# Optimization experiments

Measured on AMD Instinct MI355X. Metric: run time of the kernel, lower is better.

Reference implementation:

```python
import jax, jax.numpy as jnp
import numpy as np

N_NODES = 100000


def _gcn_conv(x, W, b, src, dst, norm):
    # x: [N, Fin] -> [N, Fout]; PyG GCNConv: linear, normalized scatter-add, bias
    x = x @ W
    msgs = x[src] * norm[:, None]  # gather + edge scale
    out = jax.ops.segment_sum(msgs, dst, num_segments=N_NODES)
    return out + b


def setup_inputs() -> dict:
    key = jax.random.key(0)
    ks = jax.random.split(key, 8)
    N, E, F, H, C = N_NODES, 600000, 128, 128, 40
    s = lambda fan: 1.0 / np.sqrt(fan)
    return {
        "features": jax.random.normal(ks[0], (N, F), dtype=jnp.float32),
        "edge_index": jax.random.randint(ks[1], (2, E), 0, N, dtype=jnp.int64),
        "W1": jax.random.normal(ks[2], (F, H), dtype=jnp.float32) * s(F),
        "b1": jnp.zeros((H,), dtype=jnp.float32),
        "W2": jax.random.normal(ks[3], (H, H), dtype=jnp.float32) * s(H),
        "b2": jnp.zeros((H,), dtype=jnp.float32),
        "W3": jax.random.normal(ks[4], (H, C), dtype=jnp.float32) * s(H),
        "b3": jnp.zeros((C,), dtype=jnp.float32),
    }


def reference(features, edge_index, W1, b1, W2, b2, W3, b3):
    N = N_NODES
    # add self-loops (PyG GCNConv default)
    loops = jnp.arange(N, dtype=edge_index.dtype)
    src = jnp.concatenate([edge_index[0], loops])
    dst = jnp.concatenate([edge_index[1], loops])
    # symmetric normalization: deg^-1/2[src] * deg^-1/2[dst]
    deg = jax.ops.segment_sum(jnp.ones_like(dst, dtype=features.dtype), dst,
                              num_segments=N)
    dis = jnp.where(deg > 0, jax.lax.rsqrt(jnp.maximum(deg, 1.0)), 0.0)
    norm = dis[src] * dis[dst]

    x = jax.nn.relu(_gcn_conv(features, W1, b1, src, dst, norm))
    x = jax.nn.relu(_gcn_conv(x, W2, b2, src, dst, norm))
    x = jax.nn.relu(_gcn_conv(x, W3, b3, src, dst, norm))
    return jax.nn.log_softmax(x, axis=-1)
```

## Files before the change

### kernel.cpp

```cpp
#include <hip/hip_runtime.h>
#include <hip/hip_bf16.h>

#define NN 100000
#define NE 600000
#define NBLK 391
#define NPAD 100096

typedef unsigned int uint;
typedef unsigned short ushort;
typedef __attribute__((ext_vector_type(8))) short bf16x8;
typedef __attribute__((ext_vector_type(4))) float f32x4;

__device__ __forceinline__ ushort f2b(float f) {
    union { float f; uint u; } v; v.f = f;
    return (ushort)((v.u + 0x7fffu + ((v.u >> 16) & 1u)) >> 16);
}
__device__ __forceinline__ uint f2b2(float lo, float hi) {
    return (uint)f2b(lo) | ((uint)f2b(hi) << 16);
}
__device__ __forceinline__ float b2f(uint h) {
    union { uint u; float f; } v; v.u = h << 16; return v.f;
}

__global__ __launch_bounds__(256) void k_cnt_init(int* __restrict__ cnt) {
    int i = blockIdx.x * 256 + threadIdx.x;
    if (i < NN) cnt[i] = 0;
}
__global__ __launch_bounds__(256) void k_cnt(const int* __restrict__ dst,
                                             int* __restrict__ cnt) {
    int e = blockIdx.x * 256 + threadIdx.x;
    if (e < NE) atomicAdd(&cnt[dst[e]], 1);
}
__global__ __launch_bounds__(256) void k_blockred(const int* __restrict__ cnt,
                                                  int* __restrict__ blocksum) {
    int t = threadIdx.x;
    int i = blockIdx.x * 256 + t;
    int c = (i < NN) ? cnt[i] : 0;
    #pragma unroll
    for (int o = 32; o; o >>= 1) c += __shfl_xor(c, o, 64);
    __shared__ int ws[4];
    if ((t & 63) == 0) ws[t >> 6] = c;
    __syncthreads();
    if (t == 0) blocksum[blockIdx.x] = ws[0] + ws[1] + ws[2] + ws[3];
}
__global__ __launch_bounds__(256) void k_scanblk_castW(const int* __restrict__ blocksum,
                                                       int* __restrict__ blockbase,
                                                       const float* __restrict__ W1,
                                                       const float* __restrict__ W2,
                                                       const float* __restrict__ W3,
                                                       ushort* __restrict__ WTall) {
    int t = threadIdx.x;
    if (blockIdx.x == 0) {
        __shared__ int s[NBLK];
        for (int i = t; i < NBLK; i += 256) s[i] = blocksum[i];
        __syncthreads();
        if (t == 0) {
            int run = 0;
            for (int i = 0; i < NBLK; ++i) { int v = s[i]; s[i] = run; run += v; }
        }
        __syncthreads();
        for (int i = t; i < NBLK; i += 256) blockbase[i] = s[i];
    } else {
        int o = (blockIdx.x - 1) * 256 + t;
        if (o >= 38912) return;
        float v;
        if (o < 32768) {
            const float* W = (o < 16384) ? W1 : W2;
            int off = o & 16383;
            int n = off >> 7, k = off & 127;
            v = W[k * 128 + n];
        } else {
            int off = o - 32768;
            int n = off >> 7, k = off & 127;
            v = (n < 40) ? W3[k * 40 + n] : 0.f;
        }
        WTall[o] = f2b(v);
    }
}
__global__ __launch_bounds__(256) void k_offsets(const int* __restrict__ cnt,
                                                 const int* __restrict__ blockbase,
                                                 int* __restrict__ offsets,
                                                 int* __restrict__ cursor,
                                                 float* __restrict__ dis) {
    int t = threadIdx.x, lane = t & 63, wv = t >> 6;
    int i = blockIdx.x * 256 + t;
    int c = (i < NN) ? cnt[i] : 0;
    int x = c;
    #pragma unroll
    for (int o = 1; o < 64; o <<= 1) {
        int v = __shfl_up(x, o, 64);
        if (lane >= o) x += v;
    }
    __shared__ int wsum[4], wbase[4];
    if (lane == 63) wsum[wv] = x;
    __syncthreads();
    if (t == 0) {
        int run = 0;
        #pragma unroll
        for (int k = 0; k < 4; ++k) { wbase[k] = run; run += wsum[k]; }
    }
    __syncthreads();
    int excl = blockbase[blockIdx.x] + wbase[wv] + x - c;
    if (i < NN) {
        offsets[i] = excl;
        cursor[i] = excl;
        dis[i] = rsqrtf((float)(c + 1));
        if (i == NN - 1) offsets[NN] = excl + c;
    }
}
__global__ __launch_bounds__(256) void k_fill(const int* __restrict__ src,
                                              const int* __restrict__ dst,
                                              const float* __restrict__ dis,
                                              int* __restrict__ cursor,
                                              int2* __restrict__ edges) {
    int e = blockIdx.x * 256 + threadIdx.x;
    if (e < NE) {
        int s = src[e], d = dst[e];
        int pos = atomicAdd(&cursor[d], 1);
        float nr = dis[s] * dis[d];
        edges[pos] = make_int2(s, __float_as_int(nr));
    }
}

template <bool F32IN>
__global__ __launch_bounds__(256) void k_gemm128b(const void* __restrict__ Xin,
                                                  const ushort* __restrict__ WT,
                                                  ushort* __restrict__ Yb) {
    __shared__ ushort AL[64 * 136];
    __shared__ ushort BL[128 * 136];
    const int t = threadIdx.x;
    const int rbase = blockIdx.x * 64;
    #pragma unroll
    for (int i = 0; i < 8; ++i) {
        int ch = t + 256 * i;
        int n = ch >> 4, c = ch & 15;
        *(int4*)(BL + n * 136 + c * 8) = *(const int4*)(WT + n * 128 + c * 8);
    }
    #pragma unroll
    for (int i = 0; i < 4; ++i) {
        int ch = t + 256 * i;
        int m = ch >> 4, c = ch & 15;
        int row = min(rbase + m, NN - 1);
        if (F32IN) {
            const float* Xf = (const float*)Xin;
            float4 f0 = *(const float4*)(Xf + (size_t)row * 128 + c * 8);
            float4 f1 = *(const float4*)(Xf + (size_t)row * 128 + c * 8 + 4);
            uint4 o;
            o.x = f2b2(f0.x, f0.y);
            o.y = f2b2(f0.z, f0.w);
            o.z = f2b2(f1.x, f1.y);
            o.w = f2b2(f1.z, f1.w);
            *(uint4*)(AL + m * 136 + c * 8) = o;
        } else {
            const ushort* Xb = (const ushort*)Xin;
            *(int4*)(AL + m * 136 + c * 8) =
                *(const int4*)(Xb + (size_t)row * 128 + c * 8);
        }
    }
    __syncthreads();
    const int wv = t >> 6, l = t & 63;
    const int m16 = l & 15, q = l >> 4;
    f32x4 acc[8];
    #pragma unroll
    for (int j = 0; j < 8; ++j) acc[j] = (f32x4){0.f, 0.f, 0.f, 0.f};
    #pragma unroll
    for (int kt = 0; kt < 4; ++kt) {
        bf16x8 a = *(const bf16x8*)(AL + (wv * 16 + m16) * 136 + kt * 32 + q * 8);
        #pragma unroll
        for (int j = 0; j < 8; ++j) {
            bf16x8 b = *(const bf16x8*)(BL + (j * 16 + m16) * 136 + kt * 32 + q * 8);
            acc[j] = __builtin_amdgcn_mfma_f32_16x16x32_bf16(a, b, acc[j], 0, 0, 0);
        }
    }
    #pragma unroll
    for (int r = 0; r < 4; ++r) {
        int row = rbase + wv * 16 + q * 4 + r;
        if (row < NN) {
            #pragma unroll
            for (int j = 0; j < 8; ++j)
                Yb[(size_t)row * 128 + j * 16 + m16] = f2b(acc[j][r]);
        }
    }
}

__global__ __launch_bounds__(256) void k_gemm40b(const ushort* __restrict__ Xb,
                                                 const ushort* __restrict__ W3T,
                                                 ushort* __restrict__ Yb) {
    __shared__ ushort AL[128 * 136];
    __shared__ ushort BL[48 * 136];
    const int t = threadIdx.x;
    const int rbase = blockIdx.x * 128;
    #pragma unroll
    for (int i = 0; i < 3; ++i) {
        int ch = t + 256 * i;
        int n = ch >> 4, c = ch & 15;
        *(int4*)(BL + n * 136 + c * 8) = *(const int4*)(W3T + n * 128 + c * 8);
    }
    #pragma unroll
    for (int i = 0; i < 8; ++i) {
        int ch = t + 256 * i;
        int m = ch >> 4, c = ch & 15;
        *(int4*)(AL + m * 136 + c * 8) =
            *(const int4*)(Xb + (size_t)(rbase + m) * 128 + c * 8);
    }
    __syncthreads();
    const int wv = t >> 6, l = t & 63;
    const int m16 = l & 15, q = l >> 4;
    f32x4 acc[2][3];
    #pragma unroll
    for (int i = 0; i < 2; ++i)
        #pragma unroll
        for (int j = 0; j < 3; ++j) acc[i][j] = (f32x4){0.f, 0.f, 0.f, 0.f};
    #pragma unroll
    for (int kt = 0; kt < 4; ++kt) {
        bf16x8 a[2], b[3];
        #pragma unroll
        for (int i = 0; i < 2; ++i)
            a[i] = *(const bf16x8*)(AL + ((wv * 2 + i) * 16 + m16) * 136 + kt * 32 + q * 8);
        #pragma unroll
        for (int j = 0; j < 3; ++j)
            b[j] = *(const bf16x8*)(BL + (j * 16 + m16) * 136 + kt * 32 + q * 8);
        #pragma unroll
        for (int i = 0; i < 2; ++i)
            #pragma unroll
            for (int j = 0; j < 3; ++j)
                acc[i][j] = __builtin_amdgcn_mfma_f32_16x16x32_bf16(a[i], b[j], acc[i][j], 0, 0, 0);
    }
    #pragma unroll
    for (int i = 0; i < 2; ++i) {
        #pragma unroll
        for (int r = 0; r < 4; ++r) {
            int row = rbase + (wv * 2 + i) * 16 + q * 4 + r;
            if (row < NN) {
                #pragma unroll
                for (int j = 0; j < 3; ++j)
                    Yb[(size_t)row * 64 + j * 16 + m16] = f2b(acc[i][j][r]);
            }
        }
    }
}

__global__ __launch_bounds__(256) void k_agg128b(const int* __restrict__ offsets,
                                                 const int2* __restrict__ edges,
                                                 const float* __restrict__ dis,
                                                 const ushort* __restrict__ xw,
                                                 const float* __restrict__ bias,
                                                 ushort* __restrict__ out) {
    const int t = threadIdx.x;
    const int wv = t >> 6, lane = t & 63;
    const int hl = lane & 15;
    const int qsel = lane & 48;
    const int n = (blockIdx.x * 4 + wv) * 4 + (lane >> 4);
    const bool nvalid = n < NN;
    const int nc = nvalid ? n : NN - 1;
    const int beg = offsets[nc], end = offsets[nc + 1];
    const int deg = end - beg;
    int2 em = (hl < deg) ? edges[beg + hl] : make_int2(0, 0);
    int s_l = em.x;
    float w_l = __int_as_float(em.y);
    float d = dis[nc];
    float dd = d * d;
    uint4 v0 = ((const uint4*)(xw + (size_t)nc * 128))[hl];
    float a0 = b2f(v0.x & 0xffffu) * dd, a1 = b2f(v0.x >> 16) * dd;
    float a2 = b2f(v0.y & 0xffffu) * dd, a3 = b2f(v0.y >> 16) * dd;
    float a4 = b2f(v0.z & 0xffffu) * dd, a5 = b2f(v0.z >> 16) * dd;
    float a6 = b2f(v0.w & 0xffffu) * dd, a7 = b2f(v0.w >> 16) * dd;
    int degc = min(deg, 16);
    int m1 = max(degc, __shfl_xor(degc, 16, 64));
    int dmax = max(m1, __shfl_xor(m1, 32, 64));
    int jceil = (dmax + 7) & ~7;
    for (int j = 0; j < jceil; j += 8) {
        int s[8]; float w[8]; uint4 u[8];
        #pragma unroll
        for (int k = 0; k < 8; ++k) {
            s[k] = __shfl(s_l, qsel + j + k, 64);
            w[k] = __shfl(w_l, qsel + j + k, 64);
        }
        #pragma unroll
        for (int k = 0; k < 8; ++k)
            u[k] = ((const uint4*)(xw + (size_t)s[k] * 128))[hl];
        #pragma unroll
        for (int k = 0; k < 8; ++k) {
            a0 = fmaf(b2f(u[k].x & 0xffffu), w[k], a0);
            a1 = fmaf(b2f(u[k].x >> 16), w[k], a1);
            a2 = fmaf(b2f(u[k].y & 0xffffu), w[k], a2);
            a3 = fmaf(b2f(u[k].y >> 16), w[k], a3);
            a4 = fmaf(b2f(u[k].z & 0xffffu), w[k], a4);
            a5 = fmaf(b2f(u[k].z >> 16), w[k], a5);
            a6 = fmaf(b2f(u[k].w & 0xffffu), w[k], a6);
            a7 = fmaf(b2f(u[k].w >> 16), w[k], a7);
        }
    }
    for (int jj = beg + 16; jj < end; ++jj) {
        int2 e2 = edges[jj];
        float w = __int_as_float(e2.y);
        uint4 u = ((const uint4*)(xw + (size_t)e2.x * 128))[hl];
        a0 = fmaf(b2f(u.x & 0xffffu), w, a0);
        a1 = fmaf(b2f(u.x >> 16), w, a1);
        a2 = fmaf(b2f(u.y & 0xffffu), w, a2);
        a3 = fmaf(b2f(u.y >> 16), w, a3);
        a4 = fmaf(b2f(u.z & 0xffffu), w, a4);
        a5 = fmaf(b2f(u.z >> 16), w, a5);
        a6 = fmaf(b2f(u.w & 0xffffu), w, a6);
        a7 = fmaf(b2f(u.w >> 16), w, a7);
    }
    float4 bv0 = ((const float4*)bias)[2 * hl];
    float4 bv1 = ((const float4*)bias)[2 * hl + 1];
    a0 = fmaxf(a0 + bv0.x, 0.f); a1 = fmaxf(a1 + bv0.y, 0.f);
    a2 = fmaxf(a2 + bv0.z, 0.f); a3 = fmaxf(a3 + bv0.w, 0.f);
    a4 = fmaxf(a4 + bv1.x, 0.f); a5 = fmaxf(a5 + bv1.y, 0.f);
    a6 = fmaxf(a6 + bv1.z, 0.f); a7 = fmaxf(a7 + bv1.w, 0.f);
    if (nvalid) {
        uint4 o;
        o.x = f2b2(a0, a1);
        o.y = f2b2(a2, a3);
        o.z = f2b2(a4, a5);
        o.w = f2b2(a6, a7);
        ((uint4*)(out + (size_t)n * 128))[hl] = o;
    }
}

__global__ __launch_bounds__(256) void k_agg40_lsm(const int* __restrict__ offsets,
                                                   const int2* __restrict__ edges,
                                                   const float* __restrict__ dis,
                                                   const ushort* __restrict__ xw,
                                                   const float* __restrict__ bias,
                                                   float* __restrict__ out) {
    const int t = threadIdx.x;
    const int wv = t >> 6, lane = t & 63;
    const int hl = lane & 31;
    const int hsel = lane & 32;
    const int n = (blockIdx.x * 4 + wv) * 2 + (lane >> 5);
    const bool nvalid = n < NN;
    const int nc = nvalid ? n : NN - 1;
    const bool act = hl < 20;
    const int beg = offsets[nc], end = offsets[nc + 1];
    const int deg = end - beg;
    int2 em = (hl < deg) ? edges[beg + hl] : make_int2(0, 0);
    int s_l = em.x;
    float w_l = __int_as_float(em.y);
    float d = dis[nc];
    uint v0 = ((const uint*)(xw + (size_t)nc * 64))[hl];
    float x0 = b2f(v0 & 0xffffu) * (d * d);
    float x1 = b2f(v0 >> 16) * (d * d);
    int degc = min(deg, 32);
    int dmax = max(degc, __shfl_xor(degc, 32, 64));
    int jceil = (dmax + 7) & ~7;
    for (int j = 0; j < jceil; j += 8) {
        int s[8]; float w[8]; uint u[8];
        #pragma unroll
        for (int k = 0; k < 8; ++k) {
            s[k] = __shfl(s_l, hsel + j + k, 64);
            w[k] = __shfl(w_l, hsel + j + k, 64);
        }
        #pragma unroll
        for (int k = 0; k < 8; ++k)
            u[k] = ((const uint*)(xw + (size_t)s[k] * 64))[hl];
        #pragma unroll
        for (int k = 0; k < 8; ++k) {
            x0 = fmaf(b2f(u[k] & 0xffffu), w[k], x0);
            x1 = fmaf(b2f(u[k] >> 16), w[k], x1);
        }
    }
    for (int jj = beg + 32; jj < end; ++jj) {
        int2 e2 = edges[jj];
        float w = __int_as_float(e2.y);
        uint u = ((const uint*)(xw + (size_t)e2.x * 64))[hl];
        x0 = fmaf(b2f(u & 0xffffu), w, x0);
        x1 = fmaf(b2f(u >> 16), w, x1);
    }
    if (act) {
        float2 bv = ((const float2*)bias)[hl];
        x0 = fmaxf(x0 + bv.x, 0.f);
        x1 = fmaxf(x1 + bv.y, 0.f);
    }
    float m = act ? fmaxf(x0, x1) : -1e30f;
    #pragma unroll
    for (int o = 16; o; o >>= 1) m = fmaxf(m, __shfl_xor(m, o, 64));
    float e = act ? (expf(x0 - m) + expf(x1 - m)) : 0.f;
    #pragma unroll
    for (int o = 16; o; o >>= 1) e += __shfl_xor(e, o, 64);
    if (act && nvalid) {
        float lg = m + logf(e);
        float2 o2 = make_float2(x0 - lg, x1 - lg);
        *(float2*)(out + (size_t)n * 40 + 2 * hl) = o2;
    }
}

extern "C" void kernel_launch(void* const* d_in, const int* in_sizes, int n_in,
                              void* d_out, int out_size, void* d_ws, size_t ws_size,
                              hipStream_t stream) {
    const float* feat = (const float*)d_in[0];
    const int* ei = (const int*)d_in[1];
    const float* W1 = (const float*)d_in[2];
    const float* b1 = (const float*)d_in[3];
    const float* W2 = (const float*)d_in[4];
    const float* b2 = (const float*)d_in[5];
    const float* W3 = (const float*)d_in[6];
    const float* b3 = (const float*)d_in[7];
    const int* src = ei;
    const int* dst = ei + NE;
    float* out = (float*)d_out;

    char* w = (char*)d_ws;
    int* cnt = (int*)w;        w += 100352 * 4;
    float* dis = (float*)w;    w += 100352 * 4;
    int* offsets = (int*)w;    w += 100608 * 4;
    int* cursor = (int*)w;     w += 100352 * 4;
    int* blocksum = (int*)w;   w += 512 * 4;
    int* blockbase = (int*)w;  w += 512 * 4;
    int2* edges = (int2*)w;    w += 600064 * 8;
    ushort* WTall = (ushort*)w; w += 39168 * 2;
    ushort* W1T = WTall;
    ushort* W2T = WTall + 16384;
    ushort* W3T = WTall + 32768;
    ushort* bufYb = (ushort*)w; w += (size_t)NPAD * 128 * 2;
    ushort* bufXb = (ushort*)w; w += (size_t)NPAD * 128 * 2;
    ushort* Y40b = (ushort*)w;  w += (size_t)NPAD * 64 * 2;

    const int B = 256;
    #define CDIV(a, b) (((a) + (b) - 1) / (b))

    k_cnt_init<<<NBLK, B, 0, stream>>>(cnt);
    k_cnt<<<CDIV(NE, B), B, 0, stream>>>(dst, cnt);
    k_blockred<<<NBLK, B, 0, stream>>>(cnt, blocksum);
    k_scanblk_castW<<<1 + CDIV(38912, B), B, 0, stream>>>(blocksum, blockbase,
                                                          W1, W2, W3, WTall);
    k_offsets<<<NBLK, B, 0, stream>>>(cnt, blockbase, offsets, cursor, dis);
    k_fill<<<CDIV(NE, B), B, 0, stream>>>(src, dst, dis, cursor, edges);

    k_gemm128b<true><<<CDIV(NN, 64), B, 0, stream>>>(feat, W1T, bufYb);
    k_agg128b<<<CDIV(NN, 16), B, 0, stream>>>(offsets, edges, dis, bufYb, b1, bufXb);
    k_gemm128b<false><<<CDIV(NN, 64), B, 0, stream>>>(bufXb, W2T, bufYb);
    k_agg128b<<<CDIV(NN, 16), B, 0, stream>>>(offsets, edges, dis, bufYb, b2, bufXb);
    k_gemm40b<<<CDIV(NN, 128), B, 0, stream>>>(bufXb, W3T, Y40b);
    k_agg40_lsm<<<CDIV(NN, 8), B, 0, stream>>>(offsets, edges, dis, Y40b, b3, out);
    #undef CDIV
}
```

Baseline: 278.6 us.

## Fold source normalization into GEMM epilogue and drop per-edge weights

Factors the symmetric norm so each GEMM output row is pre-scaled by deg^-1/2 of its own node, and the destination factor is applied once after aggregation. The CSR then stores only source indices (4 bytes per edge instead of 8), so the gather loops become plain adds with no per-edge weight shuffles. CSR fill now uses the rank returned by the counting atomic instead of a second atomic cursor pass. A zero row at index NN is written so padded lanes can gather it safely. The cost is an extra rank array and a per-row dis load in the GEMM epilogues; rounding to bf16 now happens after scaling by dis, which shifts numerics slightly.

```diff
diff --git a/kernel.cpp b/kernel.cpp
--- a/kernel.cpp
+++ b/kernel.cpp
@@ -27,9 +27,10 @@
     if (i < NN) cnt[i] = 0;
 }
 __global__ __launch_bounds__(256) void k_cnt(const int* __restrict__ dst,
-                                             int* __restrict__ cnt) {
+                                             int* __restrict__ cnt,
+                                             int* __restrict__ rank) {
     int e = blockIdx.x * 256 + threadIdx.x;
-    if (e < NE) atomicAdd(&cnt[dst[e]], 1);
+    if (e < NE) rank[e] = atomicAdd(&cnt[dst[e]], 1);
 }
 __global__ __launch_bounds__(256) void k_blockred(const int* __restrict__ cnt,
                                                   int* __restrict__ blocksum) {
@@ -80,7 +81,6 @@
 __global__ __launch_bounds__(256) void k_offsets(const int* __restrict__ cnt,
                                                  const int* __restrict__ blockbase,
                                                  int* __restrict__ offsets,
-                                                 int* __restrict__ cursor,
                                                  float* __restrict__ dis) {
     int t = threadIdx.x, lane = t & 63, wv = t >> 6;
     int i = blockIdx.x * 256 + t;
@@ -103,33 +103,35 @@
     int excl = blockbase[blockIdx.x] + wbase[wv] + x - c;
     if (i < NN) {
         offsets[i] = excl;
-        cursor[i] = excl;
         dis[i] = rsqrtf((float)(c + 1));
         if (i == NN - 1) offsets[NN] = excl + c;
     }
 }
 __global__ __launch_bounds__(256) void k_fill(const int* __restrict__ src,
                                               const int* __restrict__ dst,
-                                              const float* __restrict__ dis,
-                                              int* __restrict__ cursor,
-                                              int2* __restrict__ edges) {
+                                              const int* __restrict__ rank,
+                                              const int* __restrict__ offsets,
+                                              int* __restrict__ edges) {
     int e = blockIdx.x * 256 + threadIdx.x;
     if (e < NE) {
-        int s = src[e], d = dst[e];
-        int pos = atomicAdd(&cursor[d], 1);
-        float nr = dis[s] * dis[d];
-        edges[pos] = make_int2(s, __float_as_int(nr));
+        int s = src[e], d = dst[e], r = rank[e];
+        edges[offsets[d] + r] = s;
     }
 }
 
 template <bool F32IN>
 __global__ __launch_bounds__(256) void k_gemm128b(const void* __restrict__ Xin,
                                                   const ushort* __restrict__ WT,
+                                                  const float* __restrict__ dis,
                                                   ushort* __restrict__ Yb) {
     __shared__ ushort AL[64 * 136];
     __shared__ ushort BL[128 * 136];
     const int t = threadIdx.x;
     const int rbase = blockIdx.x * 64;
+    if (blockIdx.x == 0 && t < 16) {
+        uint4 z = make_uint4(0, 0, 0, 0);
+        ((uint4*)(Yb + (size_t)NN * 128))[t] = z;
+    }
     #pragma unroll
     for (int i = 0; i < 8; ++i) {
         int ch = t + 256 * i;
@@ -176,20 +178,26 @@
     for (int r = 0; r < 4; ++r) {
         int row = rbase + wv * 16 + q * 4 + r;
         if (row < NN) {
+            float ds = dis[row];
             #pragma unroll
             for (int j = 0; j < 8; ++j)
-                Yb[(size_t)row * 128 + j * 16 + m16] = f2b(acc[j][r]);
+                Yb[(size_t)row * 128 + j * 16 + m16] = f2b(acc[j][r] * ds);
         }
     }
 }
 
 __global__ __launch_bounds__(256) void k_gemm40b(const ushort* __restrict__ Xb,
                                                  const ushort* __restrict__ W3T,
+                                                 const float* __restrict__ dis,
                                                  ushort* __restrict__ Yb) {
     __shared__ ushort AL[128 * 136];
     __shared__ ushort BL[48 * 136];
     const int t = threadIdx.x;
     const int rbase = blockIdx.x * 128;
+    if (blockIdx.x == 0 && t < 8) {
+        uint4 z = make_uint4(0, 0, 0, 0);
+        ((uint4*)(Yb + (size_t)NN * 64))[t] = z;
+    }
     #pragma unroll
     for (int i = 0; i < 3; ++i) {
         int ch = t + 256 * i;
@@ -200,8 +208,9 @@
     for (int i = 0; i < 8; ++i) {
         int ch = t + 256 * i;
         int m = ch >> 4, c = ch & 15;
+        int row = min(rbase + m, NN - 1);
         *(int4*)(AL + m * 136 + c * 8) =
-            *(const int4*)(Xb + (size_t)(rbase + m) * 128 + c * 8);
+            *(const int4*)(Xb + (size_t)row * 128 + c * 8);
     }
     __syncthreads();
     const int wv = t >> 6, l = t & 63;
@@ -232,16 +241,17 @@
         for (int r = 0; r < 4; ++r) {
             int row = rbase + (wv * 2 + i) * 16 + q * 4 + r;
             if (row < NN) {
+                float ds = dis[row];
                 #pragma unroll
                 for (int j = 0; j < 3; ++j)
-                    Yb[(size_t)row * 64 + j * 16 + m16] = f2b(acc[i][j][r]);
+                    Yb[(size_t)row * 64 + j * 16 + m16] = f2b(acc[i][j][r] * ds);
             }
         }
     }
 }
 
 __global__ __launch_bounds__(256) void k_agg128b(const int* __restrict__ offsets,
-                                                 const int2* __restrict__ edges,
+                                                 const int* __restrict__ edges,
                                                  const float* __restrict__ dis,
                                                  const ushort* __restrict__ xw,
                                                  const float* __restrict__ bias,
@@ -255,61 +265,46 @@
     const int nc = nvalid ? n : NN - 1;
     const int beg = offsets[nc], end = offsets[nc + 1];
     const int deg = end - beg;
-    int2 em = (hl < deg) ? edges[beg + hl] : make_int2(0, 0);
-    int s_l = em.x;
-    float w_l = __int_as_float(em.y);
-    float d = dis[nc];
-    float dd = d * d;
+    int s_l = (hl < deg) ? edges[beg + hl] : NN;
     uint4 v0 = ((const uint4*)(xw + (size_t)nc * 128))[hl];
-    float a0 = b2f(v0.x & 0xffffu) * dd, a1 = b2f(v0.x >> 16) * dd;
-    float a2 = b2f(v0.y & 0xffffu) * dd, a3 = b2f(v0.y >> 16) * dd;
-    float a4 = b2f(v0.z & 0xffffu) * dd, a5 = b2f(v0.z >> 16) * dd;
-    float a6 = b2f(v0.w & 0xffffu) * dd, a7 = b2f(v0.w >> 16) * dd;
+    float a0 = b2f(v0.x & 0xffffu), a1 = b2f(v0.x >> 16);
+    float a2 = b2f(v0.y & 0xffffu), a3 = b2f(v0.y >> 16);
+    float a4 = b2f(v0.z & 0xffffu), a5 = b2f(v0.z >> 16);
+    float a6 = b2f(v0.w & 0xffffu), a7 = b2f(v0.w >> 16);
     int degc = min(deg, 16);
     int m1 = max(degc, __shfl_xor(degc, 16, 64));
     int dmax = max(m1, __shfl_xor(m1, 32, 64));
     int jceil = (dmax + 7) & ~7;
     for (int j = 0; j < jceil; j += 8) {
-        int s[8]; float w[8]; uint4 u[8];
-        #pragma unroll
-        for (int k = 0; k < 8; ++k) {
-            s[k] = __shfl(s_l, qsel + j + k, 64);
-            w[k] = __shfl(w_l, qsel + j + k, 64);
-        }
+        int s[8]; uint4 u[8];
+        #pragma unroll
+        for (int k = 0; k < 8; ++k) s[k] = __shfl(s_l, qsel + j + k, 64);
         #pragma unroll
         for (int k = 0; k < 8; ++k)
             u[k] = ((const uint4*)(xw + (size_t)s[k] * 128))[hl];
         #pragma unroll
         for (int k = 0; k < 8; ++k) {
-            a0 = fmaf(b2f(u[k].x & 0xffffu), w[k], a0);
-            a1 = fmaf(b2f(u[k].x >> 16), w[k], a1);
-            a2 = fmaf(b2f(u[k].y & 0xffffu), w[k], a2);
-            a3 = fmaf(b2f(u[k].y >> 16), w[k], a3);
-            a4 = fmaf(b2f(u[k].z & 0xffffu), w[k], a4);
-            a5 = fmaf(b2f(u[k].z >> 16), w[k], a5);
-            a6 = fmaf(b2f(u[k].w & 0xffffu), w[k], a6);
-            a7 = fmaf(b2f(u[k].w >> 16), w[k], a7);
+            a0 += b2f(u[k].x & 0xffffu); a1 += b2f(u[k].x >> 16);
+            a2 += b2f(u[k].y & 0xffffu); a3 += b2f(u[k].y >> 16);
+            a4 += b2f(u[k].z & 0xffffu); a5 += b2f(u[k].z >> 16);
+            a6 += b2f(u[k].w & 0xffffu); a7 += b2f(u[k].w >> 16);
         }
     }
     for (int jj = beg + 16; jj < end; ++jj) {
-        int2 e2 = edges[jj];
-        float w = __int_as_float(e2.y);
-        uint4 u = ((const uint4*)(xw + (size_t)e2.x * 128))[hl];
-        a0 = fmaf(b2f(u.x & 0xffffu), w, a0);
-        a1 = fmaf(b2f(u.x >> 16), w, a1);
-        a2 = fmaf(b2f(u.y & 0xffffu), w, a2);
-        a3 = fmaf(b2f(u.y >> 16), w, a3);
-        a4 = fmaf(b2f(u.z & 0xffffu), w, a4);
-        a5 = fmaf(b2f(u.z >> 16), w, a5);
-        a6 = fmaf(b2f(u.w & 0xffffu), w, a6);
-        a7 = fmaf(b2f(u.w >> 16), w, a7);
-    }
+        int s2 = edges[jj];
+        uint4 u = ((const uint4*)(xw + (size_t)s2 * 128))[hl];
+        a0 += b2f(u.x & 0xffffu); a1 += b2f(u.x >> 16);
+        a2 += b2f(u.y & 0xffffu); a3 += b2f(u.y >> 16);
+        a4 += b2f(u.z & 0xffffu); a5 += b2f(u.z >> 16);
+        a6 += b2f(u.w & 0xffffu); a7 += b2f(u.w >> 16);
+    }
+    float d = dis[nc];
     float4 bv0 = ((const float4*)bias)[2 * hl];
     float4 bv1 = ((const float4*)bias)[2 * hl + 1];
-    a0 = fmaxf(a0 + bv0.x, 0.f); a1 = fmaxf(a1 + bv0.y, 0.f);
-    a2 = fmaxf(a2 + bv0.z, 0.f); a3 = fmaxf(a3 + bv0.w, 0.f);
-    a4 = fmaxf(a4 + bv1.x, 0.f); a5 = fmaxf(a5 + bv1.y, 0.f);
-    a6 = fmaxf(a6 + bv1.z, 0.f); a7 = fmaxf(a7 + bv1.w, 0.f);
+    a0 = fmaxf(fmaf(a0, d, bv0.x), 0.f); a1 = fmaxf(fmaf(a1, d, bv0.y), 0.f);
+    a2 = fmaxf(fmaf(a2, d, bv0.z), 0.f); a3 = fmaxf(fmaf(a3, d, bv0.w), 0.f);
+    a4 = fmaxf(fmaf(a4, d, bv1.x), 0.f); a5 = fmaxf(fmaf(a5, d, bv1.y), 0.f);
+    a6 = fmaxf(fmaf(a6, d, bv1.z), 0.f); a7 = fmaxf(fmaf(a7, d, bv1.w), 0.f);
     if (nvalid) {
         uint4 o;
         o.x = f2b2(a0, a1);
@@ -321,7 +316,7 @@
 }
 
 __global__ __launch_bounds__(256) void k_agg40_lsm(const int* __restrict__ offsets,
-                                                   const int2* __restrict__ edges,
+                                                   const int* __restrict__ edges,
                                                    const float* __restrict__ dis,
                                                    const ushort* __restrict__ xw,
                                                    const float* __restrict__ bias,
@@ -336,43 +331,37 @@
     const bool act = hl < 20;
     const int beg = offsets[nc], end = offsets[nc + 1];
     const int deg = end - beg;
-    int2 em = (hl < deg) ? edges[beg + hl] : make_int2(0, 0);
-    int s_l = em.x;
-    float w_l = __int_as_float(em.y);
-    float d = dis[nc];
+    int s_l = (hl < deg) ? edges[beg + hl] : NN;
     uint v0 = ((const uint*)(xw + (size_t)nc * 64))[hl];
-    float x0 = b2f(v0 & 0xffffu) * (d * d);
-    float x1 = b2f(v0 >> 16) * (d * d);
+    float x0 = b2f(v0 & 0xffffu);
+    float x1 = b2f(v0 >> 16);
     int degc = min(deg, 32);
     int dmax = max(degc, __shfl_xor(degc, 32, 64));
     int jceil = (dmax + 7) & ~7;
     for (int j = 0; j < jceil; j += 8) {
-        int s[8]; float w[8]; uint u[8];
-        #pragma unroll
-        for (int k = 0; k < 8; ++k) {
-            s[k] = __shfl(s_l, hsel + j + k, 64);
-            w[k] = __shfl(w_l, hsel + j + k, 64);
-        }
+        int s[8]; uint u[8];
+        #pragma unroll
+        for (int k = 0; k < 8; ++k) s[k] = __shfl(s_l, hsel + j + k, 64);
         #pragma unroll
         for (int k = 0; k < 8; ++k)
             u[k] = ((const uint*)(xw + (size_t)s[k] * 64))[hl];
         #pragma unroll
         for (int k = 0; k < 8; ++k) {
-            x0 = fmaf(b2f(u[k] & 0xffffu), w[k], x0);
-            x1 = fmaf(b2f(u[k] >> 16), w[k], x1);
+            x0 += b2f(u[k] & 0xffffu);
+            x1 += b2f(u[k] >> 16);
         }
     }
     for (int jj = beg + 32; jj < end; ++jj) {
-        int2 e2 = edges[jj];
-        float w = __int_as_float(e2.y);
-        uint u = ((const uint*)(xw + (size_t)e2.x * 64))[hl];
-        x0 = fmaf(b2f(u & 0xffffu), w, x0);
-        x1 = fmaf(b2f(u >> 16), w, x1);
-    }
+        int s2 = edges[jj];
+        uint u = ((const uint*)(xw + (size_t)s2 * 64))[hl];
+        x0 += b2f(u & 0xffffu);
+        x1 += b2f(u >> 16);
+    }
+    float d = dis[nc];
     if (act) {
         float2 bv = ((const float2*)bias)[hl];
-        x0 = fmaxf(x0 + bv.x, 0.f);
-        x1 = fmaxf(x1 + bv.y, 0.f);
+        x0 = fmaxf(fmaf(x0, d, bv.x), 0.f);
+        x1 = fmaxf(fmaf(x1, d, bv.y), 0.f);
     }
     float m = act ? fmaxf(x0, x1) : -1e30f;
     #pragma unroll
@@ -406,10 +395,10 @@
     int* cnt = (int*)w;        w += 100352 * 4;
     float* dis = (float*)w;    w += 100352 * 4;
     int* offsets = (int*)w;    w += 100608 * 4;
-    int* cursor = (int*)w;     w += 100352 * 4;
+    int* rank = (int*)w;       w += 600064 * 4;
     int* blocksum = (int*)w;   w += 512 * 4;
     int* blockbase = (int*)w;  w += 512 * 4;
-    int2* edges = (int2*)w;    w += 600064 * 8;
+    int* edges = (int*)w;      w += 600064 * 4;
     ushort* WTall = (ushort*)w; w += 39168 * 2;
     ushort* W1T = WTall;
     ushort* W2T = WTall + 16384;
@@ -422,18 +411,18 @@
     #define CDIV(a, b) (((a) + (b) - 1) / (b))
 
     k_cnt_init<<<NBLK, B, 0, stream>>>(cnt);
-    k_cnt<<<CDIV(NE, B), B, 0, stream>>>(dst, cnt);
+    k_cnt<<<CDIV(NE, B), B, 0, stream>>>(dst, cnt, rank);
     k_blockred<<<NBLK, B, 0, stream>>>(cnt, blocksum);
     k_scanblk_castW<<<1 + CDIV(38912, B), B, 0, stream>>>(blocksum, blockbase,
                                                           W1, W2, W3, WTall);
-    k_offsets<<<NBLK, B, 0, stream>>>(cnt, blockbase, offsets, cursor, dis);
-    k_fill<<<CDIV(NE, B), B, 0, stream>>>(src, dst, dis, cursor, edges);
-
-    k_gemm128b<true><<<CDIV(NN, 64), B, 0, stream>>>(feat, W1T, bufYb);
+    k_offsets<<<NBLK, B, 0, stream>>>(cnt, blockbase, offsets, dis);
+    k_fill<<<CDIV(NE, B), B, 0, stream>>>(src, dst, rank, offsets, edges);
+
+    k_gemm128b<true><<<CDIV(NN, 64), B, 0, stream>>>(feat, W1T, dis, bufYb);
     k_agg128b<<<CDIV(NN, 16), B, 0, stream>>>(offsets, edges, dis, bufYb, b1, bufXb);
-    k_gemm128b<false><<<CDIV(NN, 64), B, 0, stream>>>(bufXb, W2T, bufYb);
+    k_gemm128b<false><<<CDIV(NN, 64), B, 0, stream>>>(bufXb, W2T, dis, bufYb);
     k_agg128b<<<CDIV(NN, 16), B, 0, stream>>>(offsets, edges, dis, bufYb, b2, bufXb);
-    k_gemm40b<<<CDIV(NN, 128), B, 0, stream>>>(bufXb, W3T, Y40b);
+    k_gemm40b<<<CDIV(NN, 128), B, 0, stream>>>(bufXb, W3T, dis, Y40b);
     k_agg40_lsm<<<CDIV(NN, 8), B, 0, stream>>>(offsets, edges, dis, Y40b, b3, out);
     #undef CDIV
 }
```

After: 259.5 us. 1.07x faster.
